# Optimization experiments

Measured on AMD Instinct MI355X. Metric: run time of the kernel, lower is better.

Reference implementation:

```python
import jax, jax.numpy as jnp
import numpy as np

B, S, D, H = 2, 4096, 512, 4
HD = D // H          # head_dim = key_size = value_size = 128
BLK = 512            # mask_block_size (tri-block-diagonal mask)


def setup_inputs() -> dict:
    key = jax.random.key(0)
    ks = jax.random.split(key, 7)
    # tri-block-diagonal boolean mask: query block attends to itself and adjacent blocks
    blk = np.arange(S) // BLK
    mask = np.abs(blk[:, None] - blk[None, :]) <= 1
    w_scale = 1.0 / np.sqrt(D)  # ~ variance_scaling fan_in init magnitude
    return {
        "q_input": jax.random.normal(ks[0], (B, S, D), jnp.float32),
        "kv_input": jax.random.normal(ks[1], (B, S, D), jnp.float32),
        "Wq": jax.random.normal(ks[2], (D, H * HD), jnp.float32) * w_scale,
        "Wk": jax.random.normal(ks[3], (D, H * HD), jnp.float32) * w_scale,
        "Wv": jax.random.normal(ks[4], (D, H * HD), jnp.float32) * w_scale,
        "Wo": jax.random.normal(ks[5], (H * HD, D), jnp.float32) * w_scale,
        "bo": jnp.zeros((D,), jnp.float32),
        "mask": jnp.asarray(mask),
    }


def reference(q_input, kv_input, Wq, Wk, Wv, Wo, bo, mask):
    b, s, _ = q_input.shape
    # multihead projections -> [b, s, H, HD]
    q = (q_input @ Wq).reshape(b, s, H, HD)
    k = (kv_input @ Wk).reshape(b, s, H, HD)
    v = (kv_input @ Wv).reshape(b, s, H, HD)
    # normalize_q=True: scale by key_size**-0.5 (no tanh soft cap)
    q = q * (HD ** -0.5)
    # masked attention (splash attention math): [b, H, sq, sk]
    scores = jnp.einsum("bqhd,bkhd->bhqk", q, k)
    neg = jnp.finfo(scores.dtype).min
    scores = jnp.where(mask[None, None], scores, neg)
    p = jax.nn.softmax(scores, axis=-1)
    out = jnp.einsum("bhqk,bkhd->bqhd", p, v)
    out = out.reshape(b, s, H * HD)
    return out @ Wo + bo
```

## Files before the change

### kernel.cpp

```cpp
#include <hip/hip_runtime.h>
#include <hip/hip_bf16.h>

#define S_LEN 4096
#define D_MODEL 512
#define NHEADS 4
#define HEAD_DIM 128
#define BATCH 2
#define M_ROWS 8192

typedef unsigned short u16;
typedef __attribute__((ext_vector_type(8))) short bf16x8;
typedef __attribute__((ext_vector_type(4))) short bf16x4;
typedef __attribute__((ext_vector_type(4))) float f32x4;

__device__ __forceinline__ float bf2f(u16 u) {
    return __uint_as_float(((unsigned)u) << 16);
}
__device__ __forceinline__ short f2b(float f) {
    unsigned x = __float_as_uint(f);
    unsigned r = (x + 0x7fffu + ((x >> 16) & 1u)) >> 16;
    return (short)r;
}

__device__ __forceinline__ unsigned cvtpk_bf16(float lo, float hi) {
    unsigned r;
    asm("v_cvt_pk_bf16_f32 %0, %1, %2" : "=v"(r) : "v"(lo), "v"(hi));
    return r;
}

typedef __attribute__((address_space(1))) const unsigned int g_u32;
typedef __attribute__((address_space(3))) unsigned int l_u32;
__device__ __forceinline__ void gload16(const u16* g, short* l) {
    __builtin_amdgcn_global_load_lds((g_u32*)g, (l_u32*)l, 16, 0, 0);
}

__device__ __forceinline__ int detect_f32(const u16* u, int nelem, int tid, int* s_cnt) {
    if (tid == 0) *s_cnt = 0;
    __syncthreads();
    int samp = nelem < 4096 ? nelem : 4096;
    int c = 0;
    for (int i = tid; i < samp; i += 256) {
        float af = fabsf(bf2f(u[i]));
        if (af != 0.0f && (!(af <= 1e12f) || af < 1e-12f)) c++;
    }
    atomicAdd(s_cnt, c);
    __syncthreads();
    return *s_cnt > 16;
}

__global__ __launch_bounds__(256) void prep_all(const void* qin, const void* kvin,
                                                const void* w0, const void* w1,
                                                const void* w2, const void* w3,
                                                u16* qa, u16* kva, u16* wt) {
    __shared__ int s_cnt;
    __shared__ float tile[32][33];
    const int tid = threadIdx.x, bid = blockIdx.x;
    if (bid < 2048) {
        const int which = bid >> 10, chunk = bid & 1023;
        const void* src = which ? kvin : qin;
        u16* dst = which ? kva : qa;
        const int f32 = detect_f32((const u16*)src, 4194304, tid, &s_cnt);
        const size_t base = (size_t)chunk * 4096 + (size_t)tid * 16;
        if (f32) {
            const float* s = (const float*)src + base;
            short v[16];
#pragma unroll
            for (int i = 0; i < 4; i++) {
                f32x4 t = *(const f32x4*)(s + 4 * i);
                v[4 * i] = f2b(t.x); v[4 * i + 1] = f2b(t.y);
                v[4 * i + 2] = f2b(t.z); v[4 * i + 3] = f2b(t.w);
            }
            *(bf16x8*)(dst + base) = *(bf16x8*)v;
            *(bf16x8*)(dst + base + 8) = *(bf16x8*)(v + 8);
        } else {
            const u16* s = (const u16*)src + base;
            *(bf16x8*)(dst + base) = *(const bf16x8*)s;
            *(bf16x8*)(dst + base + 8) = *(const bf16x8*)(s + 8);
        }
    } else {
        const int idx = bid - 2048, wi = idx >> 8, t = idx & 255;
        const void* W = (wi == 0) ? w0 : (wi == 1) ? w1 : (wi == 2) ? w2 : w3;
        const int f32 = detect_f32((const u16*)W, 262144, tid, &s_cnt);
        const float scale = (wi == 0) ? 0.0883883476483184f : 1.0f;
        u16* Wt = wt + (size_t)wi * D_MODEL * D_MODEL;
        const int k0 = (t >> 4) * 32, n0 = (t & 15) * 32;
        const int tx = tid & 31, ty = tid >> 5;
#pragma unroll
        for (int i = 0; i < 4; i++) {
            int r = ty + 8 * i;
            long long off = (long long)(k0 + r) * D_MODEL + n0 + tx;
            float v = f32 ? ((const float*)W)[off] : bf2f(((const u16*)W)[off]);
            tile[r][tx] = v * scale;
        }
        __syncthreads();
#pragma unroll
        for (int i = 0; i < 4; i++) {
            int r = ty + 8 * i;
            Wt[(size_t)(n0 + r) * D_MODEL + k0 + tx] = (u16)f2b(tile[tx][r]);
        }
    }
}

__global__ __launch_bounds__(256) void proj_mfma(const u16* qa, const u16* kva,
                                                 const u16* wt, u16* qb, u16* kb,
                                                 u16* vbT) {
    __shared__ short As[64][72];
    __shared__ short Ws[128][72];
    const int z = blockIdx.z;
    const u16* A = (z == 0) ? qa : kva;
    const u16* Wt = wt + (size_t)z * 262144;
    const int row0 = blockIdx.x * 64, col0 = blockIdx.y * 128;
    const int tid = threadIdx.x;
    const int lane = tid & 63, wid = tid >> 6;
    const int wm = wid >> 1, wn = wid & 1;
    const int l16 = lane & 15, quad = lane >> 4;
    const int ar = tid >> 2, ak = (tid & 3) * 16;
    const int wr = tid >> 1, wk = (tid & 1) * 32;

    f32x4 acc[2][4];
#pragma unroll
    for (int i = 0; i < 2; i++)
#pragma unroll
        for (int j = 0; j < 4; j++) acc[i][j] = (f32x4){0.f, 0.f, 0.f, 0.f};

    for (int k0 = 0; k0 < D_MODEL; k0 += 64) {
        {
            const u16* ap = A + (size_t)(row0 + ar) * D_MODEL + k0 + ak;
            *(bf16x8*)&As[ar][ak] = *(const bf16x8*)ap;
            *(bf16x8*)&As[ar][ak + 8] = *(const bf16x8*)(ap + 8);
            const u16* wp = Wt + (size_t)(col0 + wr) * D_MODEL + k0 + wk;
#pragma unroll
            for (int i = 0; i < 4; i++)
                *(bf16x8*)&Ws[wr][wk + 8 * i] = *(const bf16x8*)(wp + 8 * i);
        }
        __syncthreads();
#pragma unroll
        for (int kc = 0; kc < 2; kc++) {
            bf16x8 af[2], bfr[4];
#pragma unroll
            for (int i = 0; i < 2; i++)
                af[i] = *(const bf16x8*)&As[wm * 32 + i * 16 + l16][kc * 32 + quad * 8];
#pragma unroll
            for (int j = 0; j < 4; j++)
                bfr[j] = *(const bf16x8*)&Ws[wn * 64 + j * 16 + l16][kc * 32 + quad * 8];
#pragma unroll
            for (int i = 0; i < 2; i++)
#pragma unroll
                for (int j = 0; j < 4; j++)
                    acc[i][j] = __builtin_amdgcn_mfma_f32_16x16x32_bf16(af[i], bfr[j],
                                                                       acc[i][j], 0, 0, 0);
        }
        __syncthreads();
    }
    if (z == 2) {
#pragma unroll
        for (int i = 0; i < 2; i++) {
            int grow = row0 + wm * 32 + i * 16 + quad * 4;
            int b = grow >> 12, s = grow & (S_LEN - 1);
#pragma unroll
            for (int j = 0; j < 4; j++) {
                int gcol = col0 + wn * 64 + j * 16 + l16;
                int h = gcol >> 7, d = gcol & 127;
                short v[4];
#pragma unroll
                for (int r = 0; r < 4; r++) v[r] = f2b(acc[i][j][r]);
                *(bf16x4*)&vbT[((size_t)(b * NHEADS + h) * HEAD_DIM + d) * S_LEN + s] =
                    *(bf16x4*)v;
            }
        }
    } else {
        u16* out = (z == 0) ? qb : kb;
#pragma unroll
        for (int i = 0; i < 2; i++) {
            int grow = row0 + wm * 32 + i * 16 + quad * 4;
#pragma unroll
            for (int j = 0; j < 4; j++) {
                int gcol = col0 + wn * 64 + j * 16 + l16;
                int h = gcol >> 7, d = gcol & 127;
#pragma unroll
                for (int r = 0; r < 4; r++) {
                    int row = grow + r;
                    int b = row >> 12, s = row & (S_LEN - 1);
                    out[((size_t)(b * NHEADS + h) * S_LEN + s) * HEAD_DIM + d] =
                        (u16)f2b(acc[i][j][r]);
                }
            }
        }
    }
}

__global__ __launch_bounds__(256, 3) void attn_mfma(const u16* qb, const u16* kb,
                                                    const u16* vbT, u16* op0, u16* op1,
                                                    u16* op2, float* lp) {
    __shared__ short SM[2][8192];
    __shared__ short Ps[128][40];
    const int bid = blockIdx.x;
    const int bh = bid & 7;
    const int rest = bid >> 3;
    const int qt = rest / 3;
    const int p3 = rest - qt * 3;
    const int q0 = qt << 7;
    const int qblk = q0 >> 9;
    const int kstart0 = (qblk == 0) ? 0 : ((qblk - 1) << 9);
    const int kend0 = (qblk == 7) ? S_LEN : ((qblk + 2) << 9);
    const int kcount = kend0 - kstart0;
    const int third = (kcount / 3) & ~31;
    const int rem32 = (kcount - 3 * third) >> 5;
    const int kstart = kstart0 + p3 * third + (p3 < rem32 ? p3 : rem32) * 32;
    const int klen = third + (p3 < rem32 ? 32 : 0);
    const int tid = threadIdx.x;
    const int lane = tid & 63, wid = tid >> 6;
    const int l16 = lane & 15, quad = lane >> 4;
    const u16* qp = qb + (size_t)bh * S_LEN * HEAD_DIM;
    const u16* kp = kb + (size_t)bh * S_LEN * HEAD_DIM;
    const u16* vp = vbT + (size_t)bh * HEAD_DIM * S_LEN;
    short* smf = &SM[0][0];

    size_t koff[2], voff[2];
    int sdst[2];
#pragma unroll
    for (int s = 0; s < 2; s++) {
        const int wc = wid * 2 + s;
        const int kr = wc * 4 + quad;
        koff[s] = (size_t)kr * HEAD_DIM + (size_t)((l16 ^ (kr & 7)) * 8);
        const int vr = wc * 16 + (lane >> 2);
        voff[s] = (size_t)vr * S_LEN + (size_t)(((lane & 3) ^ (vr & 3)) * 8);
        sdst[s] = wc * 512;
    }

    bf16x8 qf[2][4];
    {
#pragma unroll
        for (int c = 0; c < 4; c++)
#pragma unroll
            for (int s = 0; s < 2; s++)
                gload16(qp + (size_t)(q0 + c * 32) * HEAD_DIM + koff[s],
                        smf + c * 4096 + sdst[s]);
        __syncthreads();
#pragma unroll
        for (int i = 0; i < 2; i++)
#pragma unroll
            for (int kc = 0; kc < 4; kc++) {
                const int row = i * 16 + l16;
                const int ch = (kc * 4 + quad) ^ (row & 7);
                qf[i][kc] = *(const bf16x8*)&smf[wid * 4096 + row * 128 + ch * 8];
            }
        __syncthreads();
    }

    f32x4 o[2][8], lacc[2];
#pragma unroll
    for (int i = 0; i < 2; i++) {
        lacc[i] = (f32x4){0.f, 0.f, 0.f, 0.f};
#pragma unroll
        for (int n = 0; n < 8; n++) o[i][n] = (f32x4){0.f, 0.f, 0.f, 0.f};
    }
    bf16x8 ones;
#pragma unroll
    for (int t = 0; t < 8; t++) ones[t] = (short)0x3F80;

    {
        const u16* kt_p = kp + (size_t)kstart * HEAD_DIM;
        const u16* vt_p = vp + kstart;
#pragma unroll
        for (int s = 0; s < 2; s++) {
            gload16(kt_p + koff[s], smf + sdst[s]);
            gload16(vt_p + voff[s], smf + 4096 + sdst[s]);
        }
    }
    const int nt = klen >> 5;
    for (int t = 0; t < nt; t++) {
        const int b = t & 1;
        const short* kbuf = smf + b * 8192;
        const short* vbuf = kbuf + 4096;
        __syncthreads();
        if (t + 1 < nt) {
            const int kt = kstart + (t + 1) * 32;
            const u16* kt_p = kp + (size_t)kt * HEAD_DIM;
            const u16* vt_p = vp + kt;
            short* dbuf = smf + (b ^ 1) * 8192;
#pragma unroll
            for (int s = 0; s < 2; s++) {
                gload16(kt_p + koff[s], dbuf + sdst[s]);
                gload16(vt_p + voff[s], dbuf + 4096 + sdst[s]);
            }
        }
        f32x4 sa[2][2];
#pragma unroll
        for (int ki = 0; ki < 2; ki++)
#pragma unroll
            for (int qi = 0; qi < 2; qi++) sa[ki][qi] = (f32x4){0.f, 0.f, 0.f, 0.f};
        __builtin_amdgcn_s_setprio(1);
#pragma unroll
        for (int kc = 0; kc < 4; kc++) {
            const int ch = ((kc * 4 + quad) ^ (l16 & 7)) * 8;
            bf16x8 kf0 = *(const bf16x8*)&kbuf[l16 * 128 + ch];
            bf16x8 kf1 = *(const bf16x8*)&kbuf[(16 + l16) * 128 + ch];
#pragma unroll
            for (int qi = 0; qi < 2; qi++) {
                sa[0][qi] = __builtin_amdgcn_mfma_f32_16x16x32_bf16(kf0, qf[qi][kc], sa[0][qi], 0, 0, 0);
                sa[1][qi] = __builtin_amdgcn_mfma_f32_16x16x32_bf16(kf1, qf[qi][kc], sa[1][qi], 0, 0, 0);
            }
        }
        __builtin_amdgcn_s_setprio(0);
#pragma unroll
        for (int ki = 0; ki < 2; ki++) {
#pragma unroll
            for (int qi = 0; qi < 2; qi++) {
                const float e0 = __expf(sa[ki][qi][0] - 8.0f);
                const float e1 = __expf(sa[ki][qi][1] - 8.0f);
                const float e2 = __expf(sa[ki][qi][2] - 8.0f);
                const float e3 = __expf(sa[ki][qi][3] - 8.0f);
                uint2 pk;
                pk.x = cvtpk_bf16(e0, e1);
                pk.y = cvtpk_bf16(e2, e3);
                *(uint2*)&Ps[wid * 32 + qi * 16 + l16][ki * 16 + quad * 4] = pk;
            }
        }
        bf16x8 pf[2];
#pragma unroll
        for (int i = 0; i < 2; i++) {
            pf[i] = *(const bf16x8*)&Ps[wid * 32 + i * 16 + l16][quad * 8];
            lacc[i] = __builtin_amdgcn_mfma_f32_16x16x32_bf16(pf[i], ones, lacc[i], 0, 0, 0);
        }
        __builtin_amdgcn_s_setprio(1);
#pragma unroll
        for (int n = 0; n < 8; n++) {
            const int d = n * 16 + l16;
            bf16x8 vf = *(const bf16x8*)&vbuf[d * 32 + ((quad ^ (d & 3)) * 8)];
#pragma unroll
            for (int i = 0; i < 2; i++)
                o[i][n] = __builtin_amdgcn_mfma_f32_16x16x32_bf16(pf[i], vf, o[i][n], 0, 0, 0);
        }
        __builtin_amdgcn_s_setprio(0);
    }
    u16* op = (p3 == 0) ? op0 : (p3 == 1 ? op1 : op2);
#pragma unroll
    for (int i = 0; i < 2; i++) {
#pragma unroll
        for (int r = 0; r < 4; r++) {
            int row = wid * 32 + i * 16 + quad * 4 + r;
            size_t gq = (size_t)bh * S_LEN + q0 + row;
#pragma unroll
            for (int n = 0; n < 8; n++)
                op[gq * HEAD_DIM + n * 16 + l16] = (u16)f2b(o[i][n][r]);
            if (l16 == 0) lp[(size_t)p3 * 8 * S_LEN + gq] = lacc[i][r];
        }
    }
}

__global__ __launch_bounds__(256) void outproj_mfma(const u16* op0, const u16* op1,
                                                    const u16* op2, const float* lp,
                                                    const u16* Wt, const void* bias,
                                                    float* out) {
    __shared__ int s_cnt;
    __shared__ short As[64][72];
    __shared__ short Ws[128][72];
    const int tid = threadIdx.x;
    const int f32b = detect_f32((const u16*)bias, 512, tid, &s_cnt);
    const int row0 = blockIdx.x * 64, col0 = blockIdx.y * 128;
    const int lane = tid & 63, wid = tid >> 6;
    const int wm = wid >> 1, wn = wid & 1;
    const int l16 = lane & 15, quad = lane >> 4;
    const int sr = tid >> 2, sk = (tid & 3) * 16;
    const int wr = tid >> 1, wk = (tid & 1) * 32;
    const size_t N = (size_t)8 * S_LEN;
    const int arow = row0 + sr;
    const int ab = arow >> 12, as = arow & (S_LEN - 1);
    f32x4 acc[2][4];
#pragma unroll
    for (int i = 0; i < 2; i++)
#pragma unroll
        for (int j = 0; j < 4; j++) acc[i][j] = (f32x4){0.f, 0.f, 0.f, 0.f};

    for (int k0 = 0; k0 < D_MODEL; k0 += 64) {
        {
            const int h = (k0 + sk) >> 7, d = (k0 + sk) & 127;
            const size_t gq = (size_t)(ab * NHEADS + h) * S_LEN + as;
            float inv = 1.0f / (lp[gq] + lp[N + gq] + lp[2 * N + gq]);
            const size_t base = gq * HEAD_DIM + d;
            bf16x8 a0 = *(const bf16x8*)&op0[base];
            bf16x8 a1 = *(const bf16x8*)&op1[base];
            bf16x8 a2 = *(const bf16x8*)&op2[base];
            bf16x8 b0 = *(const bf16x8*)&op0[base + 8];
            bf16x8 b1 = *(const bf16x8*)&op1[base + 8];
            bf16x8 b2 = *(const bf16x8*)&op2[base + 8];
            short v[16];
#pragma unroll
            for (int i = 0; i < 8; i++) {
                v[i] = f2b((bf2f((u16)a0[i]) + bf2f((u16)a1[i]) + bf2f((u16)a2[i])) * inv);
                v[8 + i] = f2b((bf2f((u16)b0[i]) + bf2f((u16)b1[i]) + bf2f((u16)b2[i])) * inv);
            }
            *(bf16x8*)&As[sr][sk] = *(bf16x8*)v;
            *(bf16x8*)&As[sr][sk + 8] = *(bf16x8*)(v + 8);
        }
        {
            const u16* wp = Wt + (size_t)(col0 + wr) * D_MODEL + k0 + wk;
#pragma unroll
            for (int i = 0; i < 4; i++)
                *(bf16x8*)&Ws[wr][wk + 8 * i] = *(const bf16x8*)(wp + 8 * i);
        }
        __syncthreads();
#pragma unroll
        for (int kc = 0; kc < 2; kc++) {
            bf16x8 af[2], bfr[4];
#pragma unroll
            for (int i = 0; i < 2; i++)
                af[i] = *(const bf16x8*)&As[wm * 32 + i * 16 + l16][kc * 32 + quad * 8];
#pragma unroll
            for (int j = 0; j < 4; j++)
                bfr[j] = *(const bf16x8*)&Ws[wn * 64 + j * 16 + l16][kc * 32 + quad * 8];
#pragma unroll
            for (int i = 0; i < 2; i++)
#pragma unroll
                for (int j = 0; j < 4; j++)
                    acc[i][j] = __builtin_amdgcn_mfma_f32_16x16x32_bf16(af[i], bfr[j],
                                                                       acc[i][j], 0, 0, 0);
        }
        __syncthreads();
    }
#pragma unroll
    for (int i = 0; i < 2; i++) {
        int grow = row0 + wm * 32 + i * 16 + quad * 4;
#pragma unroll
        for (int j = 0; j < 4; j++) {
            int gcol = col0 + wn * 64 + j * 16 + l16;
            float bval = f32b ? ((const float*)bias)[gcol] : bf2f(((const u16*)bias)[gcol]);
#pragma unroll
            for (int r = 0; r < 4; r++)
                out[(size_t)(grow + r) * D_MODEL + gcol] = acc[i][j][r] + bval;
        }
    }
}

extern "C" void kernel_launch(void* const* d_in, const int* in_sizes, int n_in,
                              void* d_out, int out_size, void* d_ws, size_t ws_size,
                              hipStream_t stream) {
    (void)in_sizes; (void)out_size; (void)ws_size; (void)n_in;
    const void* q_input = d_in[0];
    const void* kv_input = d_in[1];
    const void* Wq = d_in[2];
    const void* Wk = d_in[3];
    const void* Wv = d_in[4];
    const void* Wo = d_in[5];
    const void* bo = d_in[6];

    const size_t NELEM = (size_t)M_ROWS * D_MODEL;
    u16* wt = (u16*)d_ws;
    u16* qa = wt + 4 * 262144;
    u16* kva = qa + NELEM;
    u16* qb = kva + NELEM;
    u16* kb = qb + NELEM;
    u16* vbT = kb + NELEM;
    u16* op2 = vbT + NELEM;
    float* lp = (float*)(op2 + NELEM);
    u16* op0 = qa;
    u16* op1 = kva;

    prep_all<<<3072, 256, 0, stream>>>(q_input, kv_input, Wq, Wk, Wv, Wo, qa, kva, wt);
    proj_mfma<<<dim3(128, 4, 3), 256, 0, stream>>>(qa, kva, wt, qb, kb, vbT);
    attn_mfma<<<8 * 32 * 3, 256, 0, stream>>>(qb, kb, vbT, op0, op1, op2, lp);
    outproj_mfma<<<dim3(128, 4), 256, 0, stream>>>(op0, op1, op2, lp, wt + 3 * 262144,
                                                   bo, (float*)d_out);
}
```

Baseline: 211.3 us.

## Enlarge projection GEMM tile to 128x128 with swizzled direct-to-LDS loads

The QKV projection kernel now computes 128x128 output tiles per block, so each wave holds 4x4 MFMA accumulators instead of 2x4 and the grid halves. Staging uses a gload16 helper, apparently a direct global-to-LDS load, into unpadded shared tiles with an XOR swizzle that avoids bank conflicts. MFMA sections are wrapped with s_setprio. The aim is better operand reuse and fewer load instructions, at the cost of more registers and fewer blocks (768) to fill the GPU.

```diff
diff --git a/kernel.cpp b/kernel.cpp
--- a/kernel.cpp
+++ b/kernel.cpp
@@ -104,66 +104,70 @@
 __global__ __launch_bounds__(256) void proj_mfma(const u16* qa, const u16* kva,
                                                  const u16* wt, u16* qb, u16* kb,
                                                  u16* vbT) {
-    __shared__ short As[64][72];
-    __shared__ short Ws[128][72];
+    __shared__ short As[128][64];
+    __shared__ short Ws[128][64];
     const int z = blockIdx.z;
     const u16* A = (z == 0) ? qa : kva;
     const u16* Wt = wt + (size_t)z * 262144;
-    const int row0 = blockIdx.x * 64, col0 = blockIdx.y * 128;
+    const int row0 = blockIdx.x * 128, col0 = blockIdx.y * 128;
     const int tid = threadIdx.x;
     const int lane = tid & 63, wid = tid >> 6;
     const int wm = wid >> 1, wn = wid & 1;
     const int l16 = lane & 15, quad = lane >> 4;
-    const int ar = tid >> 2, ak = (tid & 3) * 16;
-    const int wr = tid >> 1, wk = (tid & 1) * 32;
-
-    f32x4 acc[2][4];
-#pragma unroll
-    for (int i = 0; i < 2; i++)
-#pragma unroll
-        for (int j = 0; j < 4; j++) acc[i][j] = (f32x4){0.f, 0.f, 0.f, 0.f};
+
+    const int srow = lane >> 3;
+    const int schunk = (lane & 7) ^ (srow & 7);
+    const u16* abase = A + (size_t)(row0 + wid * 32 + srow) * D_MODEL + schunk * 8;
+    const u16* wbase = Wt + (size_t)(col0 + wid * 32 + srow) * D_MODEL + schunk * 8;
+    short* adst = &As[wid * 32][0];
+    short* wdst = &Ws[wid * 32][0];
+
+    f32x4 acc[4][4];
+#pragma unroll
+    for (int m = 0; m < 4; m++)
+#pragma unroll
+        for (int n = 0; n < 4; n++) acc[m][n] = (f32x4){0.f, 0.f, 0.f, 0.f};
 
     for (int k0 = 0; k0 < D_MODEL; k0 += 64) {
-        {
-            const u16* ap = A + (size_t)(row0 + ar) * D_MODEL + k0 + ak;
-            *(bf16x8*)&As[ar][ak] = *(const bf16x8*)ap;
-            *(bf16x8*)&As[ar][ak + 8] = *(const bf16x8*)(ap + 8);
-            const u16* wp = Wt + (size_t)(col0 + wr) * D_MODEL + k0 + wk;
-#pragma unroll
-            for (int i = 0; i < 4; i++)
-                *(bf16x8*)&Ws[wr][wk + 8 * i] = *(const bf16x8*)(wp + 8 * i);
-        }
-        __syncthreads();
+#pragma unroll
+        for (int i = 0; i < 4; i++) {
+            gload16(abase + (size_t)(8 * i) * D_MODEL + k0, adst + i * 512);
+            gload16(wbase + (size_t)(8 * i) * D_MODEL + k0, wdst + i * 512);
+        }
+        __syncthreads();
+        __builtin_amdgcn_s_setprio(1);
 #pragma unroll
         for (int kc = 0; kc < 2; kc++) {
-            bf16x8 af[2], bfr[4];
-#pragma unroll
-            for (int i = 0; i < 2; i++)
-                af[i] = *(const bf16x8*)&As[wm * 32 + i * 16 + l16][kc * 32 + quad * 8];
-#pragma unroll
-            for (int j = 0; j < 4; j++)
-                bfr[j] = *(const bf16x8*)&Ws[wn * 64 + j * 16 + l16][kc * 32 + quad * 8];
-#pragma unroll
-            for (int i = 0; i < 2; i++)
-#pragma unroll
-                for (int j = 0; j < 4; j++)
-                    acc[i][j] = __builtin_amdgcn_mfma_f32_16x16x32_bf16(af[i], bfr[j],
-                                                                       acc[i][j], 0, 0, 0);
-        }
+            const int ch = ((kc * 4 + quad) ^ (l16 & 7)) * 8;
+            bf16x8 af[4], bfr[4];
+#pragma unroll
+            for (int m = 0; m < 4; m++)
+                af[m] = *(const bf16x8*)&As[wm * 64 + m * 16 + l16][ch];
+#pragma unroll
+            for (int n = 0; n < 4; n++)
+                bfr[n] = *(const bf16x8*)&Ws[wn * 64 + n * 16 + l16][ch];
+#pragma unroll
+            for (int m = 0; m < 4; m++)
+#pragma unroll
+                for (int n = 0; n < 4; n++)
+                    acc[m][n] = __builtin_amdgcn_mfma_f32_16x16x32_bf16(af[m], bfr[n],
+                                                                       acc[m][n], 0, 0, 0);
+        }
+        __builtin_amdgcn_s_setprio(0);
         __syncthreads();
     }
     if (z == 2) {
 #pragma unroll
-        for (int i = 0; i < 2; i++) {
-            int grow = row0 + wm * 32 + i * 16 + quad * 4;
+        for (int m = 0; m < 4; m++) {
+            int grow = row0 + wm * 64 + m * 16 + quad * 4;
             int b = grow >> 12, s = grow & (S_LEN - 1);
 #pragma unroll
-            for (int j = 0; j < 4; j++) {
-                int gcol = col0 + wn * 64 + j * 16 + l16;
+            for (int n = 0; n < 4; n++) {
+                int gcol = col0 + wn * 64 + n * 16 + l16;
                 int h = gcol >> 7, d = gcol & 127;
                 short v[4];
 #pragma unroll
-                for (int r = 0; r < 4; r++) v[r] = f2b(acc[i][j][r]);
+                for (int r = 0; r < 4; r++) v[r] = f2b(acc[m][n][r]);
                 *(bf16x4*)&vbT[((size_t)(b * NHEADS + h) * HEAD_DIM + d) * S_LEN + s] =
                     *(bf16x4*)v;
             }
@@ -171,18 +175,18 @@
     } else {
         u16* out = (z == 0) ? qb : kb;
 #pragma unroll
-        for (int i = 0; i < 2; i++) {
-            int grow = row0 + wm * 32 + i * 16 + quad * 4;
-#pragma unroll
-            for (int j = 0; j < 4; j++) {
-                int gcol = col0 + wn * 64 + j * 16 + l16;
+        for (int m = 0; m < 4; m++) {
+            int grow = row0 + wm * 64 + m * 16 + quad * 4;
+#pragma unroll
+            for (int n = 0; n < 4; n++) {
+                int gcol = col0 + wn * 64 + n * 16 + l16;
                 int h = gcol >> 7, d = gcol & 127;
 #pragma unroll
                 for (int r = 0; r < 4; r++) {
                     int row = grow + r;
                     int b = row >> 12, s = row & (S_LEN - 1);
                     out[((size_t)(b * NHEADS + h) * S_LEN + s) * HEAD_DIM + d] =
-                        (u16)f2b(acc[i][j][r]);
+                        (u16)f2b(acc[m][n][r]);
                 }
             }
         }
@@ -458,7 +462,7 @@
     u16* op1 = kva;
 
     prep_all<<<3072, 256, 0, stream>>>(q_input, kv_input, Wq, Wk, Wv, Wo, qa, kva, wt);
-    proj_mfma<<<dim3(128, 4, 3), 256, 0, stream>>>(qa, kva, wt, qb, kb, vbT);
+    proj_mfma<<<dim3(64, 4, 3), 256, 0, stream>>>(qa, kva, wt, qb, kb, vbT);
     attn_mfma<<<8 * 32 * 3, 256, 0, stream>>>(qb, kb, vbT, op0, op1, op2, lp);
     outproj_mfma<<<dim3(128, 4), 256, 0, stream>>>(op0, op1, op2, lp, wt + 3 * 262144,
                                                    bo, (float*)d_out);
```

Result: no change. 210.8 us (median of 3 runs) (-0.3%).
